# Performance work log

Measured on AMD Instinct MI355X. Metric: run time of the kernel, lower is better.

The kernel has to match this reference:

```python
import jax, jax.numpy as jnp
import numpy as np


def _cayley(X):
    # torch orthogonal parametrization, orthogonal_map='cayley', use_trivialization=False:
    # A = tril(X,-1); A = A - A^T (skew);  Q = (I - A/2)^{-1} (I + A/2)
    n = X.shape[0]
    A = jnp.tril(X, -1)
    A = A - A.T
    I = jnp.eye(n, dtype=X.dtype)
    return jnp.linalg.solve(I - 0.5 * A, I + 0.5 * A)


def setup_inputs() -> dict:
    key = jax.random.key(0)
    ks = jax.random.split(key, 8)
    L, R = 64, 64
    B, S = 4, 2048
    x = jax.random.normal(ks[0], (B, S, L * R), dtype=jnp.float32)
    return {
        "x": x,
        "u_left": jax.random.normal(ks[1], (L, L), dtype=jnp.float32) * 0.02,
        "v_left": jax.random.normal(ks[2], (L, L), dtype=jnp.float32) * 0.02,
        "diag_left": jnp.ones((L,), dtype=jnp.float32),
        "u_right": jax.random.normal(ks[3], (R, R), dtype=jnp.float32) * 0.02,
        "v_right": jax.random.normal(ks[4], (R, R), dtype=jnp.float32) * 0.02,
        "diag_right": jnp.ones((R,), dtype=jnp.float32),
        "diag_scale": 1.0 + 0.01 * jax.random.normal(ks[5], (L * R,), dtype=jnp.float32),
    }


def reference(x, u_left, v_left, diag_left, u_right, v_right, diag_right, diag_scale):
    L = diag_left.shape[0]
    R = diag_right.shape[0]
    # SVD-composed trans matrices: M = Cayley(U) @ diag(S) @ Cayley(V)
    m_left = _cayley(u_left) @ (diag_left[:, None] * _cayley(v_left))    # [L, L]
    m_right = _cayley(u_right) @ (diag_right[:, None] * _cayley(v_right))  # [R, R]
    # add_diag: elementwise diagonal scale on hidden dim
    xs = x * diag_scale
    shp = xs.shape
    xm = xs.reshape(-1, L, R)  # [N, L, R]
    # kronecker_matmul: m_left^T @ X @ m_right
    out = jnp.einsum('il,nij,jr->nlr', m_left, xm, m_right)
    return out.reshape(shp)
```

## Files before the change

### kernel.cpp

```cpp
#include <hip/hip_runtime.h>
#include <hip/hip_bf16.h>

typedef __attribute__((ext_vector_type(8))) short short8;
typedef __attribute__((ext_vector_type(4))) short short4v;
typedef __attribute__((ext_vector_type(4))) float floatx4;

#define MFMA(a, b, c) __builtin_amdgcn_mfma_f32_16x16x32_bf16((a), (b), (c), 0, 0, 0)

__device__ __forceinline__ short f2bf(float f) {
    unsigned u = __float_as_uint(f);
    u += 0x7fffu + ((u >> 16) & 1u);
    return (short)(u >> 16);
}

__device__ __forceinline__ short8 pack_bf16(floatx4 a, floatx4 b) {
    short8 r;
    r[0] = f2bf(a.x); r[1] = f2bf(a.y); r[2] = f2bf(a.z); r[3] = f2bf(a.w);
    r[4] = f2bf(b.x); r[5] = f2bf(b.y); r[6] = f2bf(b.z); r[7] = f2bf(b.w);
    return r;
}

__device__ void cayley64(const float* __restrict__ X, const float* __restrict__ dg,
                         short* outArr, int mode,
                         short* Brow, float* Bcol, short* T0, short* T1, int tid)
{
    int i0 = (tid * 16) >> 6;
    int j0 = (tid * 16) & 63;
#pragma unroll
    for (int s = 0; s < 16; ++s) {
        int i = i0, j = j0 + s;
        float b = 0.f;
        if (i > j)      b =  0.5f * X[i * 64 + j];
        else if (i < j) b = -0.5f * X[j * 64 + i];
        Brow[i * 72 + j] = f2bf(b);
        Bcol[j * 68 + i] = b;
        T0[j * 72 + i]   = f2bf(b);
    }
    __syncthreads();

    int lane = tid & 63, w = tid >> 6, m = lane & 15, q = lane >> 4;
    int arow = (w * 16 + m) * 72;
    short8 a0 = *(const short8*)&Brow[arow + q * 8];
    short8 a1 = *(const short8*)&Brow[arow + 32 + q * 8];

    short* Tbuf[2] = {T0, T1};
    int cur = 0;
    const int NSTEP = 6;
    for (int step = 0; step < NSTEP; ++step) {
        bool last = (step == NSTEP - 1);
        short* Tr = Tbuf[cur];
        short* Tw = Tbuf[cur ^ 1];
#pragma unroll
        for (int c = 0; c < 4; ++c) {
            int coff = c * 16 + m;
            short8 b0 = *(const short8*)&Tr[coff * 72 + q * 8];
            short8 b1 = *(const short8*)&Tr[coff * 72 + 32 + q * 8];
            floatx4 acc = {0.f, 0.f, 0.f, 0.f};
            acc = MFMA(a0, b0, acc);
            acc = MFMA(a1, b1, acc);
            int row0 = w * 16 + q * 4;
            floatx4 badd = *(const floatx4*)&Bcol[coff * 68 + row0];
            floatx4 t = badd + acc;
            if (!last) {
                short4v pk = { f2bf(t.x), f2bf(t.y), f2bf(t.z), f2bf(t.w) };
                *(short4v*)&Tw[coff * 72 + row0] = pk;
            } else {
                int col = coff;
                floatx4 cv;
                cv.x = ((row0 + 0) == col ? 1.f : 0.f) + 2.f * t.x;
                cv.y = ((row0 + 1) == col ? 1.f : 0.f) + 2.f * t.y;
                cv.z = ((row0 + 2) == col ? 1.f : 0.f) + 2.f * t.z;
                cv.w = ((row0 + 3) == col ? 1.f : 0.f) + 2.f * t.w;
                if (mode == 0) {
                    outArr[(row0 + 0) * 72 + col] = f2bf(cv.x);
                    outArr[(row0 + 1) * 72 + col] = f2bf(cv.y);
                    outArr[(row0 + 2) * 72 + col] = f2bf(cv.z);
                    outArr[(row0 + 3) * 72 + col] = f2bf(cv.w);
                } else {
                    floatx4 dv = *(const floatx4*)&dg[row0];
                    short4v pk = { f2bf(cv.x * dv.x), f2bf(cv.y * dv.y),
                                   f2bf(cv.z * dv.z), f2bf(cv.w * dv.w) };
                    *(short4v*)&outArr[col * 72 + row0] = pk;
                }
            }
        }
        __syncthreads();
        cur ^= 1;
    }
}

__global__ __launch_bounds__(256) void k_prep(
        const float* __restrict__ u_l, const float* __restrict__ v_l, const float* __restrict__ dg_l,
        const float* __restrict__ u_r, const float* __restrict__ v_r, const float* __restrict__ dg_r,
        short* __restrict__ wsOut)
{
    __shared__ __align__(16) short Brow[64 * 72];
    __shared__ __align__(16) float Bcol[64 * 68];
    __shared__ __align__(16) short T0[64 * 72];
    __shared__ __align__(16) short T1[64 * 72];
    __shared__ __align__(16) short CvA[64 * 72];
    __shared__ __align__(16) short CuB[64 * 72];

    int tid = threadIdx.x;
    const float* U  = (blockIdx.x == 0) ? u_l  : u_r;
    const float* V  = (blockIdx.x == 0) ? v_l  : v_r;
    const float* DG = (blockIdx.x == 0) ? dg_l : dg_r;
    short* outT = wsOut + blockIdx.x * 4096;

    cayley64(V, DG, CvA, 1, Brow, Bcol, T0, T1, tid);
    __syncthreads();
    cayley64(U, DG, CuB, 0, Brow, Bcol, T0, T1, tid);
    __syncthreads();

    int lane = tid & 63, w = tid >> 6, m = lane & 15, q = lane >> 4;
    int arow = (w * 16 + m) * 72;
    short8 a0 = *(const short8*)&CvA[arow + q * 8];
    short8 a1 = *(const short8*)&CvA[arow + 32 + q * 8];
#pragma unroll
    for (int c = 0; c < 4; ++c) {
        short8 b0 = *(const short8*)&CuB[(c * 16 + m) * 72 + q * 8];
        short8 b1 = *(const short8*)&CuB[(c * 16 + m) * 72 + 32 + q * 8];
        floatx4 acc = {0.f, 0.f, 0.f, 0.f};
        acc = MFMA(a0, b0, acc);
        acc = MFMA(a1, b1, acc);
        int row0 = w * 16 + q * 4, col = c * 16 + m;
        outT[(row0 + 0) * 64 + col] = f2bf(acc.x);
        outT[(row0 + 1) * 64 + col] = f2bf(acc.y);
        outT[(row0 + 2) * 64 + col] = f2bf(acc.z);
        outT[(row0 + 3) * 64 + col] = f2bf(acc.w);
    }
}

#define MPW 2

__global__ __launch_bounds__(256) void k_main(
        const float* __restrict__ x, const float* __restrict__ dsc,
        const short* __restrict__ mLT, const short* __restrict__ mRT,
        float* __restrict__ out, int N)
{
    __shared__ __align__(16) short ST[4][64 * 72];

    const int tid = threadIdx.x;
    const int w = tid >> 6, lane = tid & 63, m = lane & 15, q = lane >> 4;
    short* st = ST[w];

    short8 pf[4][2], qf[4][2];
#pragma unroll
    for (int r = 0; r < 4; ++r) {
        pf[r][0] = *(const short8*)&mLT[(r * 16 + m) * 64 + q * 8];
        pf[r][1] = *(const short8*)&mLT[(r * 16 + m) * 64 + 32 + q * 8];
        qf[r][0] = *(const short8*)&mRT[(r * 16 + m) * 64 + q * 8];
        qf[r][1] = *(const short8*)&mRT[(r * 16 + m) * 64 + 32 + q * 8];
    }

    const int gw = blockIdx.x * 4 + w;
    const long n0 = (long)gw * MPW;
    if (n0 >= N) return;
    const int nmat = ((long)N - n0 >= MPW) ? MPW : (int)((long)N - n0);
    const int nch  = nmat * 4;

    const int loff = m * 64 + q * 8;
    const float* xw = x + (size_t)n0 * 4096 + loff;
    float* ow = out + (size_t)n0 * 4096;

    floatx4 cx0 = *(const floatx4*)&xw[0];
    floatx4 cx1 = *(const floatx4*)&xw[4];
    floatx4 cx2 = *(const floatx4*)&xw[32];
    floatx4 cx3 = *(const floatx4*)&xw[36];

    for (int i = 0; i < nmat; ++i) {
#pragma unroll
        for (int rt = 0; rt < 4; ++rt) {
            const int cc = i * 4 + rt;
            const bool pfok = (cc + 1 < nch);
            floatx4 nx0, nx1, nx2, nx3;
            if (pfok) {
                const float* xn = xw + (size_t)(cc + 1) * 1024;
                nx0 = *(const floatx4*)&xn[0];
                nx1 = *(const floatx4*)&xn[4];
                nx2 = *(const floatx4*)&xn[32];
                nx3 = *(const floatx4*)&xn[36];
            }
            const float* dp = dsc + rt * 1024 + loff;
            floatx4 d0 = *(const floatx4*)&dp[0];
            floatx4 d1 = *(const floatx4*)&dp[4];
            floatx4 d2 = *(const floatx4*)&dp[32];
            floatx4 d3 = *(const floatx4*)&dp[36];

            short8 a0 = pack_bf16(cx0 * d0, cx1 * d1);
            short8 a1 = pack_bf16(cx2 * d2, cx3 * d3);

#pragma unroll
            for (int c = 0; c < 4; ++c) {
                floatx4 s = {0.f, 0.f, 0.f, 0.f};
                s = MFMA(a0, qf[c][0], s);
                s = MFMA(a1, qf[c][1], s);
                short4v pk = { f2bf(s.x), f2bf(s.y), f2bf(s.z), f2bf(s.w) };
                *(short4v*)&st[(c * 16 + m) * 72 + rt * 16 + q * 4] = pk;
            }
            if (pfok) { cx0 = nx0; cx1 = nx1; cx2 = nx2; cx3 = nx3; }
        }

        float* op = ow + (size_t)i * 4096;
#pragma unroll
        for (int c2 = 0; c2 < 4; ++c2) {
            short8 b0 = *(const short8*)&st[(c2 * 16 + m) * 72 + q * 8];
            short8 b1 = *(const short8*)&st[(c2 * 16 + m) * 72 + 32 + q * 8];
            const int col = c2 * 16 + m;
#pragma unroll
            for (int r = 0; r < 4; ++r) {
                floatx4 o = {0.f, 0.f, 0.f, 0.f};
                o = MFMA(pf[r][0], b0, o);
                o = MFMA(pf[r][1], b1, o);
                const int row0 = r * 16 + q * 4;
                __builtin_nontemporal_store(o.x, &op[(row0 + 0) * 64 + col]);
                __builtin_nontemporal_store(o.y, &op[(row0 + 1) * 64 + col]);
                __builtin_nontemporal_store(o.z, &op[(row0 + 2) * 64 + col]);
                __builtin_nontemporal_store(o.w, &op[(row0 + 3) * 64 + col]);
            }
        }
    }
}

extern "C" void kernel_launch(void* const* d_in, const int* in_sizes, int n_in,
                              void* d_out, int out_size, void* d_ws, size_t ws_size,
                              hipStream_t stream) {
    const float* x    = (const float*)d_in[0];
    const float* u_l  = (const float*)d_in[1];
    const float* v_l  = (const float*)d_in[2];
    const float* dg_l = (const float*)d_in[3];
    const float* u_r  = (const float*)d_in[4];
    const float* v_r  = (const float*)d_in[5];
    const float* dg_r = (const float*)d_in[6];
    const float* dsc  = (const float*)d_in[7];
    float* out = (float*)d_out;
    short* ws  = (short*)d_ws;

    int N = in_sizes[0] / 4096;

    hipLaunchKernelGGL(k_prep, dim3(2), dim3(256), 0, stream,
                       u_l, v_l, dg_l, u_r, v_r, dg_r, ws);
    int grid = (N + MPW * 4 - 1) / (MPW * 4);
    hipLaunchKernelGGL(k_main, dim3(grid), dim3(256), 0, stream,
                       x, dsc, ws, ws + 4096, out, N);
}
```

Baseline: 271.5 us.

## Preload both matrices' inputs upfront and store outputs as float4 vectors

Each wave now loads all x data for both of its matrices into registers at the start, and the diag_scale values once, instead of prefetching one chunk at a time. The second MFMA operands are swapped so each lane holds four consecutive columns, which turns the scalar nontemporal stores into 16-byte vector stores. Launch bounds now request 4 blocks per CU. The larger register footprint (two 16-entry float4 arrays plus dsr) may cause spilling or limit occupancy, and the nontemporal store hint is dropped.

```diff
diff --git a/kernel.cpp b/kernel.cpp
--- a/kernel.cpp
+++ b/kernel.cpp
@@ -133,7 +133,41 @@
 
 #define MPW 2
 
-__global__ __launch_bounds__(256) void k_main(
+__device__ __forceinline__ void compute_mat(
+        const floatx4* xr, const floatx4* dsr,
+        const short8 (*qf)[2], const short8 (*pf)[2],
+        short* st, float* op, int m, int q)
+{
+#pragma unroll
+    for (int rt = 0; rt < 4; ++rt) {
+        short8 a0 = pack_bf16(xr[rt * 4 + 0] * dsr[rt * 4 + 0],
+                              xr[rt * 4 + 1] * dsr[rt * 4 + 1]);
+        short8 a1 = pack_bf16(xr[rt * 4 + 2] * dsr[rt * 4 + 2],
+                              xr[rt * 4 + 3] * dsr[rt * 4 + 3]);
+#pragma unroll
+        for (int c = 0; c < 4; ++c) {
+            floatx4 s = {0.f, 0.f, 0.f, 0.f};
+            s = MFMA(a0, qf[c][0], s);
+            s = MFMA(a1, qf[c][1], s);
+            short4v pk = { f2bf(s.x), f2bf(s.y), f2bf(s.z), f2bf(s.w) };
+            *(short4v*)&st[(c * 16 + m) * 72 + rt * 16 + q * 4] = pk;
+        }
+    }
+#pragma unroll
+    for (int c2 = 0; c2 < 4; ++c2) {
+        short8 sb0 = *(const short8*)&st[(c2 * 16 + m) * 72 + q * 8];
+        short8 sb1 = *(const short8*)&st[(c2 * 16 + m) * 72 + 32 + q * 8];
+#pragma unroll
+        for (int r = 0; r < 4; ++r) {
+            floatx4 o = {0.f, 0.f, 0.f, 0.f};
+            o = MFMA(sb0, pf[r][0], o);
+            o = MFMA(sb1, pf[r][1], o);
+            *(floatx4*)&op[(r * 16 + m) * 64 + c2 * 16 + q * 4] = o;
+        }
+    }
+}
+
+__global__ __launch_bounds__(256, 4) void k_main(
         const float* __restrict__ x, const float* __restrict__ dsc,
         const short* __restrict__ mLT, const short* __restrict__ mRT,
         float* __restrict__ out, int N)
@@ -153,73 +187,39 @@
         qf[r][1] = *(const short8*)&mRT[(r * 16 + m) * 64 + 32 + q * 8];
     }
 
+    const int loff = m * 64 + q * 8;
+    constexpr int co[4] = {0, 4, 32, 36};
+
+    floatx4 dsr[16];
+#pragma unroll
+    for (int rt = 0; rt < 4; ++rt) {
+        const float* dp = dsc + rt * 1024 + loff;
+#pragma unroll
+        for (int c = 0; c < 4; ++c)
+            dsr[rt * 4 + c] = *(const floatx4*)&dp[co[c]];
+    }
+
     const int gw = blockIdx.x * 4 + w;
     const long n0 = (long)gw * MPW;
     if (n0 >= N) return;
-    const int nmat = ((long)N - n0 >= MPW) ? MPW : (int)((long)N - n0);
-    const int nch  = nmat * 4;
-
-    const int loff = m * 64 + q * 8;
     const float* xw = x + (size_t)n0 * 4096 + loff;
     float* ow = out + (size_t)n0 * 4096;
 
-    floatx4 cx0 = *(const floatx4*)&xw[0];
-    floatx4 cx1 = *(const floatx4*)&xw[4];
-    floatx4 cx2 = *(const floatx4*)&xw[32];
-    floatx4 cx3 = *(const floatx4*)&xw[36];
-
-    for (int i = 0; i < nmat; ++i) {
-#pragma unroll
-        for (int rt = 0; rt < 4; ++rt) {
-            const int cc = i * 4 + rt;
-            const bool pfok = (cc + 1 < nch);
-            floatx4 nx0, nx1, nx2, nx3;
-            if (pfok) {
-                const float* xn = xw + (size_t)(cc + 1) * 1024;
-                nx0 = *(const floatx4*)&xn[0];
-                nx1 = *(const floatx4*)&xn[4];
-                nx2 = *(const floatx4*)&xn[32];
-                nx3 = *(const floatx4*)&xn[36];
-            }
-            const float* dp = dsc + rt * 1024 + loff;
-            floatx4 d0 = *(const floatx4*)&dp[0];
-            floatx4 d1 = *(const floatx4*)&dp[4];
-            floatx4 d2 = *(const floatx4*)&dp[32];
-            floatx4 d3 = *(const floatx4*)&dp[36];
-
-            short8 a0 = pack_bf16(cx0 * d0, cx1 * d1);
-            short8 a1 = pack_bf16(cx2 * d2, cx3 * d3);
-
-#pragma unroll
-            for (int c = 0; c < 4; ++c) {
-                floatx4 s = {0.f, 0.f, 0.f, 0.f};
-                s = MFMA(a0, qf[c][0], s);
-                s = MFMA(a1, qf[c][1], s);
-                short4v pk = { f2bf(s.x), f2bf(s.y), f2bf(s.z), f2bf(s.w) };
-                *(short4v*)&st[(c * 16 + m) * 72 + rt * 16 + q * 4] = pk;
-            }
-            if (pfok) { cx0 = nx0; cx1 = nx1; cx2 = nx2; cx3 = nx3; }
-        }
-
-        float* op = ow + (size_t)i * 4096;
-#pragma unroll
-        for (int c2 = 0; c2 < 4; ++c2) {
-            short8 b0 = *(const short8*)&st[(c2 * 16 + m) * 72 + q * 8];
-            short8 b1 = *(const short8*)&st[(c2 * 16 + m) * 72 + 32 + q * 8];
-            const int col = c2 * 16 + m;
-#pragma unroll
-            for (int r = 0; r < 4; ++r) {
-                floatx4 o = {0.f, 0.f, 0.f, 0.f};
-                o = MFMA(pf[r][0], b0, o);
-                o = MFMA(pf[r][1], b1, o);
-                const int row0 = r * 16 + q * 4;
-                __builtin_nontemporal_store(o.x, &op[(row0 + 0) * 64 + col]);
-                __builtin_nontemporal_store(o.y, &op[(row0 + 1) * 64 + col]);
-                __builtin_nontemporal_store(o.z, &op[(row0 + 2) * 64 + col]);
-                __builtin_nontemporal_store(o.w, &op[(row0 + 3) * 64 + col]);
-            }
-        }
-    }
+    floatx4 xa[16], xb[16];
+#pragma unroll
+    for (int c = 0; c < 16; ++c)
+        xa[c] = *(const floatx4*)&xw[(c >> 2) * 1024 + co[c & 3]];
+
+    const bool has2 = (n0 + 1 < N);
+    if (has2) {
+#pragma unroll
+        for (int c = 0; c < 16; ++c)
+            xb[c] = *(const floatx4*)&xw[4096 + (c >> 2) * 1024 + co[c & 3]];
+    }
+
+    compute_mat(xa, dsr, qf, pf, st, ow, m, q);
+    if (has2)
+        compute_mat(xb, dsr, qf, pf, st, ow + 4096, m, q);
 }
 
 extern "C" void kernel_launch(void* const* d_in, const int* in_sizes, int n_in,
```

New measurement: 368.0 us. 35.5% more time.
